# Kernel tuning notes

Hardware: AMD Instinct MI355X
Metric: run time of the kernel (lower is better)

Reference implementation:

```python
import jax, jax.numpy as jnp
import numpy as np

B, T, C = 4, 2048, 768
H, D = 12, 64          # num_heads, head_size
R = 64                 # kv_lora_rank
ROPE_THETA = 10000.0


def setup_inputs() -> dict:
    key = jax.random.key(0)
    ks = jax.random.split(key, 8)
    s = lambda fan_in: 1.0 / np.sqrt(fan_in)
    return {
        "x":      jax.random.normal(ks[0], (B, T, C), jnp.float32),
        "Wq":     jax.random.normal(ks[1], (C, H * D), jnp.float32) * s(C),
        "Wdown":  jax.random.normal(ks[2], (C, R), jnp.float32) * s(C),
        "ln_g":   jnp.ones((R,), jnp.float32),
        "ln_b":   jnp.zeros((R,), jnp.float32),
        "Wup":    jax.random.normal(ks[3], (R, 2 * H * D), jnp.float32) * s(R),
        "Wo":     jax.random.normal(ks[4], (H * D, C), jnp.float32) * s(H * D),
        "bo":     jnp.zeros((C,), jnp.float32),
    }


def _rope_cos_sin(t, d, dtype):
    # freqs over half-dim, repeated twice (rotate-half convention)
    inv_freq = 1.0 / (ROPE_THETA ** (jnp.arange(0, d, 2, dtype=jnp.float32) / d))
    ang = jnp.arange(t, dtype=jnp.float32)[:, None] * inv_freq[None, :]  # [T, D/2]
    ang = jnp.concatenate([ang, ang], axis=-1)                            # [T, D]
    return jnp.cos(ang).astype(dtype), jnp.sin(ang).astype(dtype)


def _apply_rope(q, cos, sin):
    # q: [B, H, T, D]; cos/sin: [T, D]
    d2 = q.shape[-1] // 2
    rot = jnp.concatenate([-q[..., d2:], q[..., :d2]], axis=-1)
    return q * cos + rot * sin


def reference(x, Wq, Wdown, ln_g, ln_b, Wup, Wo, bo):
    b, t, c = x.shape
    q = (x @ Wq).reshape(b, t, H, D).transpose(0, 2, 1, 3)  # [B,H,T,D]

    ckv = x @ Wdown                                         # [B,T,R]
    mu = jnp.mean(ckv, axis=-1, keepdims=True)
    var = jnp.var(ckv, axis=-1, keepdims=True)
    ckv = (ckv - mu) * jax.lax.rsqrt(var + 1e-5) * ln_g + ln_b

    kv = (ckv @ Wup).reshape(b, t, 2, H, D)
    k = kv[:, :, 0].transpose(0, 2, 1, 3)                   # [B,H,T,D]
    v = kv[:, :, 1].transpose(0, 2, 1, 3)

    cos, sin = _rope_cos_sin(t, D, x.dtype)
    q = _apply_rope(q, cos, sin)
    k = _apply_rope(k, cos, sin)

    wei = jnp.einsum("bhqd,bhkd->bhqk", q, k) * (D ** -0.5)
    causal = jnp.tril(jnp.ones((t, t), bool))
    wei = jnp.where(causal, wei, -jnp.inf)
    wei = jax.nn.softmax(wei, axis=-1)                      # dropout: eval mode (identity)

    out = jnp.einsum("bhqk,bhkd->bhqd", wei, v)             # [B,H,T,D]
    out = out.transpose(0, 2, 1, 3).reshape(b, t, H * D)
    return out @ Wo + bo
```

## Files before the change

kernel.cpp:

```cpp
#include <hip/hip_runtime.h>
#include <hip/hip_bf16.h>
#include <math.h>

#define B_ 4
#define T_ 2048
#define C_ 768
#define H_ 12
#define D_ 64
#define R_ 64
#define BT_ (B_*T_)
#define HD_ (H_*D_)

typedef __attribute__((ext_vector_type(8))) short bf16x8;
typedef __attribute__((ext_vector_type(4))) float f32x4;

__device__ inline short f2bf(float f) {
  union { float f; unsigned u; } x; x.f = f;
  unsigned r = x.u + 0x7fffu + ((x.u >> 16) & 1u);
  return (short)(r >> 16);
}
__device__ inline unsigned pk_bf16(float a, float b) {
#if __has_builtin(__builtin_amdgcn_cvt_pk_bf16_f32)
  auto t = __builtin_amdgcn_cvt_pk_bf16_f32(a, b);
  unsigned u; __builtin_memcpy(&u, &t, sizeof(unsigned)); return u;
#else
  union { float f; unsigned u; } x, y; x.f = a; y.f = b;
  unsigned ra = (x.u + 0x7fffu + ((x.u >> 16) & 1u)) >> 16;
  unsigned rb = (y.u + 0x7fffu + ((y.u >> 16) & 1u)) & 0xffff0000u;
  return ra | rb;
#endif
}
__device__ inline float fexp2(float x) {
#if __has_builtin(__builtin_amdgcn_exp2f)
  return __builtin_amdgcn_exp2f(x);
#else
  return exp2f(x);
#endif
}
typedef __attribute__((address_space(3))) unsigned lds_u32;
typedef __attribute__((address_space(1))) const unsigned glb_u32;
__device__ inline void gload_lds16(const void* g, void* l) {
  __builtin_amdgcn_global_load_lds((glb_u32*)g, (lds_u32*)l, 16, 0, 0);
}

__global__ void convert_f32_bf16(const float* __restrict__ in, short* __restrict__ out, int n4) {
  int i = blockIdx.x * blockDim.x + threadIdx.x;
  if (i < n4) {
    float4 v = ((const float4*)in)[i];
    short4 o;
    o.x = f2bf(v.x); o.y = f2bf(v.y); o.z = f2bf(v.z); o.w = f2bf(v.w);
    ((short4*)out)[i] = o;
  }
}

__device__ inline void ttile(const float* __restrict__ src, short* __restrict__ dst,
                             int K, int N, int k0, int n0, int tid, float (*tl)[33]) {
  int tx = tid & 31, ty = tid >> 5;
  #pragma unroll
  for (int r = 0; r < 4; ++r)
    tl[ty + 8 * r][tx] = src[(size_t)(k0 + ty + 8 * r) * N + n0 + tx];
  __syncthreads();
  #pragma unroll
  for (int r = 0; r < 4; ++r)
    dst[(size_t)(n0 + ty + 8 * r) * K + k0 + tx] = f2bf(tl[tx][ty + 8 * r]);
}

__global__ __launch_bounds__(256) void prep_all(
    const float* __restrict__ Wq, const float* __restrict__ Wd,
    const float* __restrict__ Wup, const float* __restrict__ Wo,
    short* __restrict__ W1T, short* __restrict__ WupT, short* __restrict__ WoT,
    float* __restrict__ cs, float* __restrict__ sn) {
  __shared__ float tl[32][33];
  int blk = blockIdx.x, tid = threadIdx.x;
  if (blk < 576) {
    int tk = blk % 24, tn = blk / 24;
    ttile(Wq, W1T, 768, 768, tk * 32, tn * 32, tid, tl);
  } else if (blk < 624) {
    int l = blk - 576; int tk = l % 24, tn = l / 24;
    ttile(Wd, W1T + (size_t)768 * 768, 768, 64, tk * 32, tn * 32, tid, tl);
  } else if (blk < 720) {
    int l = blk - 624; int tk = l % 2, tn = l / 2;
    ttile(Wup, WupT, 64, 1536, tk * 32, tn * 32, tid, tl);
  } else if (blk < 1296) {
    int l = blk - 720; int tk = l % 24, tn = l / 24;
    ttile(Wo, WoT, 768, 768, tk * 32, tn * 32, tid, tl);
  } else {
    int base = (blk - 1296) * 1024;
    #pragma unroll
    for (int i = 0; i < 4; ++i) {
      int idx = base + tid + i * 256;
      int j = idx & 31, t = idx >> 5;
      float invf = exp2f(-(float)j * (13.287712379549449f / 32.f));
      float a = (float)t * invf;
      cs[idx] = cosf(a);
      sn[idx] = sinf(a);
    }
  }
}

#define SC2_ 0.18033688f

template<int MODE>
__global__ __launch_bounds__(256) void gemm64(
    const short* __restrict__ A, const short* __restrict__ Bt,
    int M, int N, int K,
    float* __restrict__ out0, const float* __restrict__ bias,
    const float* __restrict__ bias2,
    short* __restrict__ ob0, short* __restrict__ ob1,
    const float* __restrict__ cs, const float* __restrict__ sn)
{
  __shared__ short SM[128 * 64 + 64 * 64];
  short* As = SM;
  short* Bs = SM + 128 * 64;
  const int m0 = blockIdx.x * 128;
  const int n0 = blockIdx.y * 64;
  const int tid = threadIdx.x, lane = tid & 63, w = tid >> 6;
  const int fr = lane & 15, fk = (lane >> 4) * 8;
  const int rstage = lane >> 3;
  const int cstage = (lane & 7) * 8;

  f32x4 acc[2][4] = {};

  for (int k0 = 0; k0 < K; k0 += 64) {
    __syncthreads();
    #pragma unroll
    for (int i = 0; i < 4; ++i) {
      int c = w * 4 + i;
      int r = c * 8 + rstage;
      gload_lds16(&A[(size_t)(m0 + r) * K + k0 + cstage], &As[c * 512]);
    }
    #pragma unroll
    for (int i = 0; i < 2; ++i) {
      int c = w * 2 + i;
      int r = c * 8 + rstage;
      gload_lds16(&Bt[(size_t)(n0 + r) * K + k0 + cstage], &Bs[c * 512]);
    }
    __syncthreads();
    #pragma unroll
    for (int kk = 0; kk < 64; kk += 32) {
      bf16x8 a[2], b[4];
      a[0] = *(const bf16x8*)&As[(w * 32 +      fr) * 64 + kk + fk];
      a[1] = *(const bf16x8*)&As[(w * 32 + 16 + fr) * 64 + kk + fk];
      #pragma unroll
      for (int ni = 0; ni < 4; ++ni)
        b[ni] = *(const bf16x8*)&Bs[(ni * 16 + fr) * 64 + kk + fk];
      #pragma unroll
      for (int mi = 0; mi < 2; ++mi)
        #pragma unroll
        for (int ni = 0; ni < 4; ++ni)
          acc[mi][ni] = __builtin_amdgcn_mfma_f32_16x16x32_bf16(a[mi], b[ni], acc[mi][ni], 0, 0, 0);
    }
  }

  const int er = (lane >> 4) * 4, ec = lane & 15;

  if constexpr (MODE == 2) {
    #pragma unroll
    for (int mi = 0; mi < 2; ++mi)
      #pragma unroll
      for (int r = 0; r < 4; ++r) {
        int row = m0 + w * 32 + mi * 16 + er + r;
        #pragma unroll
        for (int ni = 0; ni < 4; ++ni) {
          int col = n0 + ni * 16 + ec;
          out0[(size_t)row * N + col] = acc[mi][ni][r] + bias[col];
        }
      }
    return;
  }

  if (n0 < 768) {
    int h = n0 >> 6;
    #pragma unroll
    for (int mi = 0; mi < 2; ++mi)
      #pragma unroll
      for (int r = 0; r < 4; ++r) {
        int row = m0 + w * 32 + mi * 16 + er + r;
        int t = row & (T_ - 1), bb = row >> 11;
        short* dst = ob0 + (((size_t)(bb * H_ + h)) * T_ + t) * 64;
        #pragma unroll
        for (int ni = 0; ni < 2; ++ni) {
          int d = ni * 16 + ec;
          float c = cs[t * 32 + d], s = sn[t * 32 + d];
          if constexpr (MODE == 0) { c *= SC2_; s *= SC2_; }
          float x0 = acc[mi][ni][r], x1 = acc[mi][ni + 2][r];
          dst[d]      = f2bf(x0 * c - x1 * s);
          dst[d + 32] = f2bf(x1 * c + x0 * s);
        }
      }
  } else if constexpr (MODE == 0) {
    #pragma unroll
    for (int mi = 0; mi < 2; ++mi)
      #pragma unroll
      for (int r = 0; r < 4; ++r) {
        float s = 0.f, s2 = 0.f;
        #pragma unroll
        for (int ni = 0; ni < 4; ++ni) { float v = acc[mi][ni][r]; s += v; s2 += v*v; }
        #pragma unroll
        for (int off = 1; off < 16; off <<= 1) {
          s  += __shfl_xor(s, off);
          s2 += __shfl_xor(s2, off);
        }
        float mu = s * (1.f/64.f);
        float var = s2 * (1.f/64.f) - mu * mu;
        float rstd = rsqrtf(var + 1e-5f);
        int row = m0 + w * 32 + mi * 16 + er + r;
        #pragma unroll
        for (int ni = 0; ni < 4; ++ni) {
          int d = ni * 16 + ec;
          ob1[(size_t)row * 64 + d] = f2bf((acc[mi][ni][r] - mu) * rstd * bias[d] + bias2[d]);
        }
      }
  } else {
    __syncthreads();
    short* Wl = SM + w * 2560;
    int h = (n0 - 768) >> 6;
    #pragma unroll
    for (int mi = 0; mi < 2; ++mi) {
      int tl0 = mi * 16 + er;
      #pragma unroll
      for (int ni = 0; ni < 4; ++ni) {
        int d = ni * 16 + ec;
        uint2 uu;
        uu.x = pk_bf16(acc[mi][ni][0], acc[mi][ni][1]);
        uu.y = pk_bf16(acc[mi][ni][2], acc[mi][ni][3]);
        *(uint2*)&Wl[d * 40 + tl0] = uu;
      }
    }
    int bb = m0 >> 11;
    int tg0 = (m0 & (T_ - 1)) + w * 32;
    int dl = lane >> 2, tl = (lane & 3) * 8;
    #pragma unroll
    for (int j = 0; j < 4; ++j) {
      int d = j * 16 + dl;
      uint4 vv = *(const uint4*)&Wl[d * 40 + tl];
      *(uint4*)&ob1[((size_t)(bb * H_ + h) * 64 + d) * T_ + tg0 + tl] = vv;
    }
  }
}

__global__ __launch_bounds__(256) void attn_mfma(
    const short* __restrict__ qgl, const short* __restrict__ kg,
    const short* __restrict__ vtg, short* __restrict__ o)
{
  __shared__ short Ks[8 * 512];
  __shared__ short Vts[8 * 512];
  __shared__ short Ps[4][1184];

  const int bh = blockIdx.x;
  const int y  = blockIdx.y;
  const int qt1 = 31 - y, qt2 = y;
  const int tid = threadIdx.x, lane = tid & 63, w = tid >> 6;
  const int q16 = lane & 15, quad = lane >> 4;
  short* Pw = Ps[w];
  const short* kb  = kg  + (size_t)bh * T_ * 64;
  const short* vtb = vtg + (size_t)bh * 64 * T_;
  const int b = bh / H_, h = bh - b * H_;

  const int qbase[2] = {qt1 * 64 + w * 16, qt2 * 64 + w * 16};
  bf16x8 bq[2][2];
  #pragma unroll
  for (int g = 0; g < 2; ++g) {
    const short* qrow = qgl + ((size_t)bh * T_ + qbase[g] + q16) * 64;
    bq[g][0] = *(const bf16x8*)&qrow[quad * 8];
    bq[g][1] = *(const bf16x8*)&qrow[32 + quad * 8];
  }

  f32x4 oacc[2][4] = {};
  float lrun[2] = {0.f, 0.f};
  const int last  = qt1 * 64;
  const int last2 = qt2 * 64;

  for (int kt = 0; kt <= last; kt += 64) {
    __syncthreads();
    #pragma unroll
    for (int i = 0; i < 2; ++i) {
      int c = w * 2 + i;
      int s = c >> 1, ch = c & 1;
      gload_lds16(kb  + (size_t)(kt + s * 16 + q16) * 64 + ch * 32 + quad * 8, &Ks[c * 512]);
      gload_lds16(vtb + (size_t)(s * 16 + q16) * T_ + kt + ch * 32 + quad * 8, &Vts[c * 512]);
    }
    __syncthreads();

    bf16x8 ak[4][2];
    #pragma unroll
    for (int s = 0; s < 4; ++s) {
      ak[s][0] = *(const bf16x8*)&Ks[(s * 2 + 0) * 512 + lane * 8];
      ak[s][1] = *(const bf16x8*)&Ks[(s * 2 + 1) * 512 + lane * 8];
    }

    #pragma unroll
    for (int g = 0; g < 2; ++g) {
      if (g == 1 && kt > last2) break;
      const int diag_end = (g == 0) ? last : last2;
      const int qidx = qbase[g] + q16;

      f32x4 sacc[4];
      #pragma unroll
      for (int s = 0; s < 4; ++s) {
        f32x4 t0 = {};
        t0 = __builtin_amdgcn_mfma_f32_16x16x32_bf16(ak[s][0], bq[g][0], t0, 0, 0, 0);
        t0 = __builtin_amdgcn_mfma_f32_16x16x32_bf16(ak[s][1], bq[g][1], t0, 0, 0, 0);
        sacc[s] = t0;
      }

      float pv[16];
      float ls = 0.f;
      if (kt != diag_end) {
        #pragma unroll
        for (int s = 0; s < 4; ++s)
          #pragma unroll
          for (int r = 0; r < 4; ++r) {
            float p = fexp2(sacc[s][r]);
            pv[s * 4 + r] = p; ls += p;
          }
      } else {
        #pragma unroll
        for (int s = 0; s < 4; ++s)
          #pragma unroll
          for (int r = 0; r < 4; ++r) {
            int key = kt + s * 16 + quad * 4 + r;
            float p = (key <= qidx) ? fexp2(sacc[s][r]) : 0.f;
            pv[s * 4 + r] = p; ls += p;
          }
      }
      ls += __shfl_xor(ls, 16);
      ls += __shfl_xor(ls, 32);
      lrun[g] += ls;

      #pragma unroll
      for (int s = 0; s < 4; ++s) {
        uint2 uu;
        uu.x = pk_bf16(pv[s * 4 + 0], pv[s * 4 + 1]);
        uu.y = pk_bf16(pv[s * 4 + 2], pv[s * 4 + 3]);
        *(uint2*)&Pw[q16 * 72 + s * 16 + quad * 4] = uu;
      }

      #pragma unroll
      for (int c = 0; c < 2; ++c) {
        bf16x8 bp = *(const bf16x8*)&Pw[q16 * 72 + c * 32 + quad * 8];
        #pragma unroll
        for (int ms = 0; ms < 4; ++ms) {
          bf16x8 av = *(const bf16x8*)&Vts[(ms * 2 + c) * 512 + lane * 8];
          oacc[g][ms] = __builtin_amdgcn_mfma_f32_16x16x32_bf16(av, bp, oacc[g][ms], 0, 0, 0);
        }
      }
    }
  }

  #pragma unroll
  for (int g = 0; g < 2; ++g) {
    float inv = 1.f / lrun[g];
    #pragma unroll
    for (int ms = 0; ms < 4; ++ms) {
      uint2 uu;
      uu.x = pk_bf16(oacc[g][ms][0] * inv, oacc[g][ms][1] * inv);
      uu.y = pk_bf16(oacc[g][ms][2] * inv, oacc[g][ms][3] * inv);
      *(uint2*)&Pw[q16 * 72 + ms * 16 + quad * 4] = uu;
    }
    int row = lane >> 2, cc2 = (lane & 3) * 16;
    uint4 r0 = *(const uint4*)&Pw[row * 72 + cc2];
    uint4 r1 = *(const uint4*)&Pw[row * 72 + cc2 + 8];
    int t = qbase[g] + row;
    short* orow = o + ((size_t)(b * T_ + t)) * HD_ + h * 64 + cc2;
    *(uint4*)&orow[0] = r0;
    *(uint4*)&orow[8] = r1;
  }
}

extern "C" void kernel_launch(void* const* d_in, const int* in_sizes, int n_in,
                              void* d_out, int out_size, void* d_ws, size_t ws_size,
                              hipStream_t stream) {
  (void)in_sizes; (void)n_in; (void)out_size; (void)ws_size;
  const float* x     = (const float*)d_in[0];
  const float* Wq    = (const float*)d_in[1];
  const float* Wdown = (const float*)d_in[2];
  const float* ln_g  = (const float*)d_in[3];
  const float* ln_b  = (const float*)d_in[4];
  const float* Wup   = (const float*)d_in[5];
  const float* Wo    = (const float*)d_in[6];
  const float* bo    = (const float*)d_in[7];
  float* out = (float*)d_out;

  char* w = (char*)d_ws;
  short* x_bf   = (short*)w;  w += (size_t)BT_ * C_    * 2;
  short* W1T    = (short*)w;  w += (size_t)832 * C_    * 2;
  short* WupT   = (short*)w;  w += (size_t)2*HD_ * R_  * 2;
  short* WoT    = (short*)w;  w += (size_t)HD_ * C_    * 2;
  short* ckv    = (short*)w;  w += (size_t)BT_ * R_    * 2;
  short* qb     = (short*)w;  w += (size_t)BT_ * HD_   * 2;
  short* kb     = (short*)w;  w += (size_t)BT_ * HD_   * 2;
  short* vt     = (short*)w;  w += (size_t)BT_ * HD_   * 2;
  short* att    = (short*)w;  w += (size_t)BT_ * HD_   * 2;
  float* cs_t   = (float*)w;  w += (size_t)T_ * 32 * 4;
  float* sn_t   = (float*)w;  w += (size_t)T_ * 32 * 4;

  prep_all<<<1360, 256, 0, stream>>>(Wq, Wdown, Wup, Wo, W1T, WupT, WoT, cs_t, sn_t);
  convert_f32_bf16<<<(BT_*C_/4 + 255)/256, 256, 0, stream>>>(x, x_bf, BT_*C_/4);

  gemm64<0><<<dim3(BT_/128, 13), 256, 0, stream>>>(
      x_bf, W1T, BT_, 832, C_, nullptr, ln_g, ln_b, qb, ckv, cs_t, sn_t);

  gemm64<1><<<dim3(BT_/128, 24), 256, 0, stream>>>(
      ckv, WupT, BT_, 2*HD_, R_, nullptr, nullptr, nullptr, kb, vt, cs_t, sn_t);

  attn_mfma<<<dim3(B_*H_, 16), 256, 0, stream>>>(qb, kb, vt, att);

  gemm64<2><<<dim3(BT_/128, 12), 256, 0, stream>>>(
      att, WoT, BT_, C_, HD_, out, bo, nullptr, nullptr, nullptr, nullptr, nullptr);
}
```

Before: 223.2 us.

## Switch attention to 32x32 MFMA with per-wave query tiles; fuse conversion into prep

The attention kernel now gives each wave 32 query rows from one of the two paired query tiles and uses 32x32x16 bf16 MFMAs instead of 16x16x32. This raises the work per MFMA and cuts LDS reads and redundant K fragment loads. On the diagonal it skips the fully masked key half. Separately, the x fp32-to-bf16 conversion is merged into the weight-prep kernel, saving one launch. The trade-off is imbalance: waves working on the shorter query tile sit idle for later key tiles while still joining the barriers.

```diff
diff --git a/kernel.cpp b/kernel.cpp
--- a/kernel.cpp
+++ b/kernel.cpp
@@ -13,6 +13,7 @@
 
 typedef __attribute__((ext_vector_type(8))) short bf16x8;
 typedef __attribute__((ext_vector_type(4))) float f32x4;
+typedef __attribute__((ext_vector_type(16))) float f32x16;
 
 __device__ inline short f2bf(float f) {
   union { float f; unsigned u; } x; x.f = f;
@@ -43,16 +44,6 @@
   __builtin_amdgcn_global_load_lds((glb_u32*)g, (lds_u32*)l, 16, 0, 0);
 }
 
-__global__ void convert_f32_bf16(const float* __restrict__ in, short* __restrict__ out, int n4) {
-  int i = blockIdx.x * blockDim.x + threadIdx.x;
-  if (i < n4) {
-    float4 v = ((const float4*)in)[i];
-    short4 o;
-    o.x = f2bf(v.x); o.y = f2bf(v.y); o.z = f2bf(v.z); o.w = f2bf(v.w);
-    ((short4*)out)[i] = o;
-  }
-}
-
 __device__ inline void ttile(const float* __restrict__ src, short* __restrict__ dst,
                              int K, int N, int k0, int n0, int tid, float (*tl)[33]) {
   int tx = tid & 31, ty = tid >> 5;
@@ -65,13 +56,25 @@
     dst[(size_t)(n0 + ty + 8 * r) * K + k0 + tx] = f2bf(tl[tx][ty + 8 * r]);
 }
 
-__global__ __launch_bounds__(256) void prep_all(
+#define NCONV (BT_*C_/4/256)
+
+__global__ __launch_bounds__(256) void prep_conv(
+    const float* __restrict__ x, short* __restrict__ x_bf,
     const float* __restrict__ Wq, const float* __restrict__ Wd,
     const float* __restrict__ Wup, const float* __restrict__ Wo,
     short* __restrict__ W1T, short* __restrict__ WupT, short* __restrict__ WoT,
     float* __restrict__ cs, float* __restrict__ sn) {
   __shared__ float tl[32][33];
-  int blk = blockIdx.x, tid = threadIdx.x;
+  int tid = threadIdx.x;
+  if (blockIdx.x < NCONV) {
+    int i = blockIdx.x * 256 + tid;
+    float4 v = ((const float4*)x)[i];
+    short4 o;
+    o.x = f2bf(v.x); o.y = f2bf(v.y); o.z = f2bf(v.z); o.w = f2bf(v.w);
+    ((short4*)x_bf)[i] = o;
+    return;
+  }
+  int blk = blockIdx.x - NCONV;
   if (blk < 576) {
     int tk = blk % 24, tn = blk / 24;
     ttile(Wq, W1T, 768, 768, tk * 32, tn * 32, tid, tl);
@@ -245,126 +248,110 @@
 {
   __shared__ short Ks[8 * 512];
   __shared__ short Vts[8 * 512];
-  __shared__ short Ps[4][1184];
+  __shared__ short Ps[4][32 * 72];
 
   const int bh = blockIdx.x;
   const int y  = blockIdx.y;
   const int qt1 = 31 - y, qt2 = y;
   const int tid = threadIdx.x, lane = tid & 63, w = tid >> 6;
-  const int q16 = lane & 15, quad = lane >> 4;
+  const int q32 = lane & 31, half = lane >> 5;
   short* Pw = Ps[w];
   const short* kb  = kg  + (size_t)bh * T_ * 64;
   const short* vtb = vtg + (size_t)bh * 64 * T_;
   const int b = bh / H_, h = bh - b * H_;
 
-  const int qbase[2] = {qt1 * 64 + w * 16, qt2 * 64 + w * 16};
-  bf16x8 bq[2][2];
-  #pragma unroll
-  for (int g = 0; g < 2; ++g) {
-    const short* qrow = qgl + ((size_t)bh * T_ + qbase[g] + q16) * 64;
-    bq[g][0] = *(const bf16x8*)&qrow[quad * 8];
-    bq[g][1] = *(const bf16x8*)&qrow[32 + quad * 8];
-  }
-
-  f32x4 oacc[2][4] = {};
-  float lrun[2] = {0.f, 0.f};
-  const int last  = qt1 * 64;
-  const int last2 = qt2 * 64;
-
-  for (int kt = 0; kt <= last; kt += 64) {
+  const int qt_w = (w < 2) ? qt1 : qt2;
+  const int q0 = qt_w * 64 + (w & 1) * 32;
+  const int last_w = qt_w * 64;
+  const int qidx = q0 + q32;
+
+  const short* qrow = qgl + ((size_t)bh * T_ + qidx) * 64;
+  bf16x8 bq[4];
+  #pragma unroll
+  for (int ks = 0; ks < 4; ++ks)
+    bq[ks] = *(const bf16x8*)&qrow[ks * 16 + half * 8];
+
+  f32x16 oacc[2] = {};
+  float lrun = 0.f;
+  const int kend = qt1 * 64;
+
+  for (int kt = 0; kt <= kend; kt += 64) {
     __syncthreads();
     #pragma unroll
     for (int i = 0; i < 2; ++i) {
       int c = w * 2 + i;
-      int s = c >> 1, ch = c & 1;
-      gload_lds16(kb  + (size_t)(kt + s * 16 + q16) * 64 + ch * 32 + quad * 8, &Ks[c * 512]);
-      gload_lds16(vtb + (size_t)(s * 16 + q16) * T_ + kt + ch * 32 + quad * 8, &Vts[c * 512]);
-    }
-    __syncthreads();
-
-    bf16x8 ak[4][2];
-    #pragma unroll
-    for (int s = 0; s < 4; ++s) {
-      ak[s][0] = *(const bf16x8*)&Ks[(s * 2 + 0) * 512 + lane * 8];
-      ak[s][1] = *(const bf16x8*)&Ks[(s * 2 + 1) * 512 + lane * 8];
-    }
-
-    #pragma unroll
-    for (int g = 0; g < 2; ++g) {
-      if (g == 1 && kt > last2) break;
-      const int diag_end = (g == 0) ? last : last2;
-      const int qidx = qbase[g] + q16;
-
-      f32x4 sacc[4];
-      #pragma unroll
-      for (int s = 0; s < 4; ++s) {
-        f32x4 t0 = {};
-        t0 = __builtin_amdgcn_mfma_f32_16x16x32_bf16(ak[s][0], bq[g][0], t0, 0, 0, 0);
-        t0 = __builtin_amdgcn_mfma_f32_16x16x32_bf16(ak[s][1], bq[g][1], t0, 0, 0, 0);
-        sacc[s] = t0;
-      }
-
+      int kh = c >> 2, ks = c & 3;
+      gload_lds16(kb + (size_t)(kt + kh * 32 + q32) * 64 + ks * 16 + half * 8, &Ks[c * 512]);
+      gload_lds16(vtb + (size_t)(kh * 32 + q32) * T_ + kt + ks * 16 + half * 8, &Vts[c * 512]);
+    }
+    __syncthreads();
+
+    if (kt > last_w) continue;
+    const bool diag = (kt == last_w);
+    const int dkh = diag ? (w & 1) : 2;
+    const bool skip1 = diag && ((w & 1) == 0);
+
+    float ls = 0.f;
+    #pragma unroll
+    for (int kh = 0; kh < 2; ++kh) {
+      if (kh == 1 && skip1) break;
+      f32x16 sacc = {};
+      #pragma unroll
+      for (int ks = 0; ks < 4; ++ks) {
+        bf16x8 a = *(const bf16x8*)&Ks[(kh * 4 + ks) * 512 + lane * 8];
+        sacc = __builtin_amdgcn_mfma_f32_32x32x16_bf16(a, bq[ks], sacc, 0, 0, 0);
+      }
       float pv[16];
-      float ls = 0.f;
-      if (kt != diag_end) {
-        #pragma unroll
-        for (int s = 0; s < 4; ++s)
-          #pragma unroll
-          for (int r = 0; r < 4; ++r) {
-            float p = fexp2(sacc[s][r]);
-            pv[s * 4 + r] = p; ls += p;
-          }
+      if (kh != dkh) {
+        #pragma unroll
+        for (int r = 0; r < 16; ++r) { float p = fexp2(sacc[r]); pv[r] = p; ls += p; }
       } else {
         #pragma unroll
-        for (int s = 0; s < 4; ++s)
-          #pragma unroll
-          for (int r = 0; r < 4; ++r) {
-            int key = kt + s * 16 + quad * 4 + r;
-            float p = (key <= qidx) ? fexp2(sacc[s][r]) : 0.f;
-            pv[s * 4 + r] = p; ls += p;
-          }
-      }
-      ls += __shfl_xor(ls, 16);
-      ls += __shfl_xor(ls, 32);
-      lrun[g] += ls;
-
-      #pragma unroll
-      for (int s = 0; s < 4; ++s) {
+        for (int r = 0; r < 16; ++r) {
+          int key = kt + kh * 32 + (r & 3) + 8 * (r >> 2) + 4 * half;
+          float p = (key <= qidx) ? fexp2(sacc[r]) : 0.f;
+          pv[r] = p; ls += p;
+        }
+      }
+      #pragma unroll
+      for (int g2 = 0; g2 < 4; ++g2) {
         uint2 uu;
-        uu.x = pk_bf16(pv[s * 4 + 0], pv[s * 4 + 1]);
-        uu.y = pk_bf16(pv[s * 4 + 2], pv[s * 4 + 3]);
-        *(uint2*)&Pw[q16 * 72 + s * 16 + quad * 4] = uu;
-      }
-
-      #pragma unroll
-      for (int c = 0; c < 2; ++c) {
-        bf16x8 bp = *(const bf16x8*)&Pw[q16 * 72 + c * 32 + quad * 8];
-        #pragma unroll
-        for (int ms = 0; ms < 4; ++ms) {
-          bf16x8 av = *(const bf16x8*)&Vts[(ms * 2 + c) * 512 + lane * 8];
-          oacc[g][ms] = __builtin_amdgcn_mfma_f32_16x16x32_bf16(av, bp, oacc[g][ms], 0, 0, 0);
-        }
-      }
-    }
-  }
-
-  #pragma unroll
-  for (int g = 0; g < 2; ++g) {
-    float inv = 1.f / lrun[g];
-    #pragma unroll
-    for (int ms = 0; ms < 4; ++ms) {
+        uu.x = pk_bf16(pv[4 * g2 + 0], pv[4 * g2 + 1]);
+        uu.y = pk_bf16(pv[4 * g2 + 2], pv[4 * g2 + 3]);
+        *(uint2*)&Pw[q32 * 72 + kh * 32 + 8 * g2 + 4 * half] = uu;
+      }
+    }
+    ls += __shfl_xor(ls, 32);
+    lrun += ls;
+
+    const int ksmax = skip1 ? 2 : 4;
+    for (int ks = 0; ks < ksmax; ++ks) {
+      bf16x8 bp = *(const bf16x8*)&Pw[q32 * 72 + ks * 16 + half * 8];
+      #pragma unroll
+      for (int dt = 0; dt < 2; ++dt) {
+        bf16x8 av = *(const bf16x8*)&Vts[(dt * 4 + ks) * 512 + lane * 8];
+        oacc[dt] = __builtin_amdgcn_mfma_f32_32x32x16_bf16(av, bp, oacc[dt], 0, 0, 0);
+      }
+    }
+  }
+
+  float inv = 1.f / lrun;
+  #pragma unroll
+  for (int dt = 0; dt < 2; ++dt)
+    #pragma unroll
+    for (int g2 = 0; g2 < 4; ++g2) {
       uint2 uu;
-      uu.x = pk_bf16(oacc[g][ms][0] * inv, oacc[g][ms][1] * inv);
-      uu.y = pk_bf16(oacc[g][ms][2] * inv, oacc[g][ms][3] * inv);
-      *(uint2*)&Pw[q16 * 72 + ms * 16 + quad * 4] = uu;
-    }
-    int row = lane >> 2, cc2 = (lane & 3) * 16;
-    uint4 r0 = *(const uint4*)&Pw[row * 72 + cc2];
-    uint4 r1 = *(const uint4*)&Pw[row * 72 + cc2 + 8];
-    int t = qbase[g] + row;
-    short* orow = o + ((size_t)(b * T_ + t)) * HD_ + h * 64 + cc2;
-    *(uint4*)&orow[0] = r0;
-    *(uint4*)&orow[8] = r1;
+      uu.x = pk_bf16(oacc[dt][4 * g2 + 0] * inv, oacc[dt][4 * g2 + 1] * inv);
+      uu.y = pk_bf16(oacc[dt][4 * g2 + 2] * inv, oacc[dt][4 * g2 + 3] * inv);
+      *(uint2*)&Pw[q32 * 72 + dt * 32 + 8 * g2 + 4 * half] = uu;
+    }
+  int row = lane >> 1, seg = lane & 1;
+  int t = q0 + row;
+  short* orow = o + ((size_t)(b * T_ + t)) * HD_ + h * 64 + seg * 32;
+  #pragma unroll
+  for (int i = 0; i < 4; ++i) {
+    uint4 vv = *(const uint4*)&Pw[row * 72 + seg * 32 + i * 8];
+    *(uint4*)&orow[i * 8] = vv;
   }
 }
 
@@ -395,8 +382,8 @@
   float* cs_t   = (float*)w;  w += (size_t)T_ * 32 * 4;
   float* sn_t   = (float*)w;  w += (size_t)T_ * 32 * 4;
 
-  prep_all<<<1360, 256, 0, stream>>>(Wq, Wdown, Wup, Wo, W1T, WupT, WoT, cs_t, sn_t);
-  convert_f32_bf16<<<(BT_*C_/4 + 255)/256, 256, 0, stream>>>(x, x_bf, BT_*C_/4);
+  prep_conv<<<NCONV + 1360, 256, 0, stream>>>(x, x_bf, Wq, Wdown, Wup, Wo,
+                                              W1T, WupT, WoT, cs_t, sn_t);
 
   gemm64<0><<<dim3(BT_/128, 13), 256, 0, stream>>>(
       x_bf, W1T, BT_, 832, C_, nullptr, ln_g, ln_b, qb, ckv, cs_t, sn_t);
```

Result: faster. 205.8 us (-7.8%).
